# Performance work log

Hardware: AMD Instinct MI355X
Metric: run time of the kernel (lower is better)

Reference implementation:

```python
import jax, jax.numpy as jnp
import numpy as np

ALPHA = 0.2  # LeakyReLU negative slope


def setup_inputs() -> dict:
    key = jax.random.key(0)
    ks = jax.random.split(key, 7)
    B, Wn, K, E, O = 16, 64, 256, 128, 64
    s = lambda k, shape, fan: jax.random.normal(k, shape, jnp.float32) * (1.0 / np.sqrt(fan))
    return {
        "x": jax.random.normal(ks[0], (B, Wn, K), jnp.float32),
        "lin_w": s(ks[1], (E, 2 * Wn), 2 * Wn),   # torch Linear weight (out,in)
        "lin_b": jnp.zeros((E,), jnp.float32),
        "a": s(ks[2], (E,), E),
        "bias_kk": s(ks[3], (K, K), K) * 0.1,
        "fc_w": s(ks[4], (O, K), K),
        "fc_b": jnp.zeros((O,), jnp.float32),
    }


def reference(x, lin_w, lin_b, a, bias_kk, fc_w, fc_b):
    # x: (B, W, K) -> v: (B, K, W); K nodes, W features per node
    v = jnp.transpose(x, (0, 2, 1))
    Wn = v.shape[-1]
    # lin(concat(v_i, v_j)) == v_i @ W1^T + v_j @ W2^T + b  (avoids O(K^2*2W) concat)
    W1, W2 = lin_w[:, :Wn], lin_w[:, Wn:]
    left = jnp.einsum("bkw,ew->bke", v, W1)   # (B,K,E)
    right = jnp.einsum("bkw,ew->bke", v, W2)  # (B,K,E)
    g = left[:, :, None, :] + right[:, None, :, :] + lin_b  # (B,K,K,E)
    g = jnp.where(g >= 0, g, ALPHA * g)  # LeakyReLU
    e = jnp.einsum("bije,e->bij", g, a) + bias_kk  # (B,K,K)
    attn = jax.nn.softmax(e, axis=2)
    # dropout p=0.0 / eval mode -> identity
    h = jax.nn.sigmoid(jnp.einsum("bij,bjw->biw", attn, v))  # (B,K,W)
    out = jnp.einsum("bwk,ok->bwo", jnp.transpose(h, (0, 2, 1)), fc_w) + fc_b
    return out  # (B, W, out_dim)
```

## Files before the change

### kernel.cpp

```cpp
#include <hip/hip_runtime.h>
#include <hip/hip_bf16.h>

#define ALPHA 0.2f
#define C1 0.6f
#define C2 0.4f

typedef const __attribute__((address_space(1))) float gas_float;
typedef __attribute__((address_space(3))) float las_float;

__device__ __forceinline__ void gld_lds16(const float* g, float* l) {
  __builtin_amdgcn_global_load_lds((gas_float*)g, (las_float*)l, 16, 0, 0);
}

__global__ __launch_bounds__(256) void k_proj(
    const float* __restrict__ x, const float* __restrict__ lin_w,
    float* __restrict__ left, float* __restrict__ right, float* __restrict__ v) {
  const int xcd = blockIdx.x & 7;
  const int s   = blockIdx.x >> 3;
  const int b   = 2 * xcd + (s & 1);
  const int k0  = (s >> 1) * 8;
  const int tid = threadIdx.x;

  __shared__ float s_x[8][68];

  {
    const int w  = tid >> 2;
    const int kq = tid & 3;
    float2 xv = *(const float2*)(x + b * 16384 + w * 256 + k0 + kq * 2);
    s_x[kq * 2 + 0][w] = xv.x;
    s_x[kq * 2 + 1][w] = xv.y;
  }
  __syncthreads();

  if (tid < 128) {
    const int k  = tid >> 4;
    const int wq = tid & 15;
    float4 vv = *(const float4*)&s_x[k][wq * 4];
    *(float4*)(v + (b * 256 + k0 + k) * 64 + wq * 4) = vv;
  }

  const int e  = tid & 127;
  const int kh = tid >> 7;
  float accL[4] = {0, 0, 0, 0};
  float accR[4] = {0, 0, 0, 0};
  const float4* w1 = (const float4*)(lin_w + e * 128);
  const float4* w2 = w1 + 16;
#pragma unroll
  for (int wc = 0; wc < 16; ++wc) {
    float4 l = w1[wc];
    float4 r = w2[wc];
#pragma unroll
    for (int k = 0; k < 4; ++k) {
      float4 sx = *(const float4*)&s_x[kh * 4 + k][wc * 4];
      accL[k] += sx.x * l.x + sx.y * l.y + sx.z * l.z + sx.w * l.w;
      accR[k] += sx.x * r.x + sx.y * r.y + sx.z * r.z + sx.w * r.w;
    }
  }
#pragma unroll
  for (int k = 0; k < 4; ++k) {
    int kk = (b * 256 + k0 + kh * 4 + k) * 128 + e;
    left[kk]  = accL[k];
    right[kk] = accR[k];
  }
}

__global__ __launch_bounds__(256, 2) void k_attn(
    const float* __restrict__ left, const float* __restrict__ right,
    const float* __restrict__ lin_b, const float* __restrict__ a,
    const float* __restrict__ bias_kk, const float* __restrict__ v,
    float* __restrict__ h) {
  const int xcd = blockIdx.x & 7;
  const int sblk = blockIdx.x >> 3;
  const int b   = 2 * xcd + (sblk & 1);
  const int i0  = (sblk >> 1) * 8;
  const int tid = threadIdx.x;

  __shared__ float s_lb[8][132];
  __shared__ float s_a[128];
  __shared__ float s_ca[128];
  __shared__ float s_AL[8];
  __shared__ float s_sc[8][260];
  __shared__ float s_v[256][64];

  float bk[8];
#pragma unroll
  for (int i = 0; i < 8; ++i) bk[i] = bias_kk[(i0 + i) * 256 + tid];

  if (tid < 128) {
    float av = a[tid];
    s_a[tid]  = av;
    s_ca[tid] = C2 * av;
  }
  {
    const int ii = tid >> 5;
    const int e4 = (tid & 31) * 4;
    float4 lv = *(const float4*)(left + (b * 256 + i0 + ii) * 128 + e4);
    float4 bv = *(const float4*)(lin_b + e4);
    lv.x += bv.x; lv.y += bv.y; lv.z += bv.z; lv.w += bv.w;
    *(float4*)&s_lb[ii][e4] = lv;
  }
  __syncthreads();

  const float4* rp = (const float4*)(right + (b * 256 + tid) * 128);
  float4 r[32];
#pragma unroll
  for (int q = 0; q < 32; ++q) r[q] = rp[q];

  {
    const int seg0 = (tid >> 6) * 16;
    const int ln4  = (tid & 63) * 4;
    const float* vb = v + b * 16384;
#pragma unroll
    for (int t = 0; t < 16; ++t) {
      const int seg = seg0 + t;
      gld_lds16(vb + seg * 256 + ln4, &s_v[0][0] + seg * 256);
    }
  }

  {
    const int ii = tid >> 5, sl = tid & 31;
    float p = 0.f;
#pragma unroll
    for (int m = 0; m < 4; ++m) p += s_a[sl * 4 + m] * s_lb[ii][sl * 4 + m];
#pragma unroll
    for (int off = 16; off > 0; off >>= 1) p += __shfl_xor(p, off, 64);
    if (sl == 0) s_AL[ii] = p;
  }

  float acc[8];
#pragma unroll
  for (int i = 0; i < 8; ++i) acc[i] = 0.f;
  float ar = 0.f;
#pragma unroll
  for (int ec = 0; ec < 8; ++ec) {
    float4 r0 = r[ec * 4 + 0], r1 = r[ec * 4 + 1],
           r2 = r[ec * 4 + 2], r3 = r[ec * 4 + 3];
    float4 a0 = *(const float4*)&s_a[ec * 16 + 0];
    float4 a1 = *(const float4*)&s_a[ec * 16 + 4];
    float4 a2 = *(const float4*)&s_a[ec * 16 + 8];
    float4 a3 = *(const float4*)&s_a[ec * 16 + 12];
    ar += a0.x * r0.x + a0.y * r0.y + a0.z * r0.z + a0.w * r0.w;
    ar += a1.x * r1.x + a1.y * r1.y + a1.z * r1.z + a1.w * r1.w;
    ar += a2.x * r2.x + a2.y * r2.y + a2.z * r2.z + a2.w * r2.w;
    ar += a3.x * r3.x + a3.y * r3.y + a3.z * r3.z + a3.w * r3.w;
    float4 c0 = *(const float4*)&s_ca[ec * 16 + 0];
    float4 c1 = *(const float4*)&s_ca[ec * 16 + 4];
    float4 c2 = *(const float4*)&s_ca[ec * 16 + 8];
    float4 c3 = *(const float4*)&s_ca[ec * 16 + 12];
#pragma unroll
    for (int i = 0; i < 8; ++i) {
      float4 l0 = *(const float4*)&s_lb[i][ec * 16 + 0];
      float4 l1 = *(const float4*)&s_lb[i][ec * 16 + 4];
      float4 l2 = *(const float4*)&s_lb[i][ec * 16 + 8];
      float4 l3 = *(const float4*)&s_lb[i][ec * 16 + 12];
      float t, s = acc[i];
      t = l0.x + r0.x; s = fmaf(c0.x, fabsf(t), s);
      t = l0.y + r0.y; s = fmaf(c0.y, fabsf(t), s);
      t = l0.z + r0.z; s = fmaf(c0.z, fabsf(t), s);
      t = l0.w + r0.w; s = fmaf(c0.w, fabsf(t), s);
      t = l1.x + r1.x; s = fmaf(c1.x, fabsf(t), s);
      t = l1.y + r1.y; s = fmaf(c1.y, fabsf(t), s);
      t = l1.z + r1.z; s = fmaf(c1.z, fabsf(t), s);
      t = l1.w + r1.w; s = fmaf(c1.w, fabsf(t), s);
      t = l2.x + r2.x; s = fmaf(c2.x, fabsf(t), s);
      t = l2.y + r2.y; s = fmaf(c2.y, fabsf(t), s);
      t = l2.z + r2.z; s = fmaf(c2.z, fabsf(t), s);
      t = l2.w + r2.w; s = fmaf(c2.w, fabsf(t), s);
      t = l3.x + r3.x; s = fmaf(c3.x, fabsf(t), s);
      t = l3.y + r3.y; s = fmaf(c3.y, fabsf(t), s);
      t = l3.z + r3.z; s = fmaf(c3.z, fabsf(t), s);
      t = l3.w + r3.w; s = fmaf(c3.w, fabsf(t), s);
      acc[i] = s;
    }
  }
  __syncthreads();

#pragma unroll
  for (int i = 0; i < 8; ++i) {
    float sc = fmaf(C1, s_AL[i] + ar, acc[i]) + bk[i];
    s_sc[i][tid] = __expf(sc);
  }
  __syncthreads();

  float invA, invB;
  {
    const int wv = tid >> 6, lane = tid & 63;
    float sA = s_sc[2 * wv + 0][lane] + s_sc[2 * wv + 0][lane + 64] +
               s_sc[2 * wv + 0][lane + 128] + s_sc[2 * wv + 0][lane + 192];
    float sB = s_sc[2 * wv + 1][lane] + s_sc[2 * wv + 1][lane + 64] +
               s_sc[2 * wv + 1][lane + 128] + s_sc[2 * wv + 1][lane + 192];
#pragma unroll
    for (int off = 32; off > 0; off >>= 1) {
      sA += __shfl_xor(sA, off, 64);
      sB += __shfl_xor(sB, off, 64);
    }
    invA = 1.f / sA;
    invB = 1.f / sB;
  }

  const int iq = tid >> 5;
  const int w  = (tid & 31) * 2;
  float h0 = 0.f, h1 = 0.f;
#pragma unroll 4
  for (int jj = 0; jj < 256; jj += 4) {
    float4 at = *(const float4*)&s_sc[iq][jj];
    float2 v0 = *(const float2*)&s_v[jj + 0][w];
    float2 v1 = *(const float2*)&s_v[jj + 1][w];
    float2 v2 = *(const float2*)&s_v[jj + 2][w];
    float2 v3 = *(const float2*)&s_v[jj + 3][w];
    h0 += at.x * v0.x + at.y * v1.x + at.z * v2.x + at.w * v3.x;
    h1 += at.x * v0.y + at.y * v1.y + at.z * v2.y + at.w * v3.y;
  }
  const float inv = (iq & 1) ? invB : invA;
  float2 hv;
  hv.x = 1.f / (1.f + __expf(-h0 * inv));
  hv.y = 1.f / (1.f + __expf(-h1 * inv));
  *(float2*)(h + (b * 256 + i0 + iq) * 64 + w) = hv;
}

__global__ __launch_bounds__(256) void k_out(
    const float* __restrict__ h, const float* __restrict__ fc_w,
    const float* __restrict__ fc_b, float* __restrict__ out) {
  const int xcd = blockIdx.x & 7;
  const int s   = blockIdx.x >> 3;
  const int b   = 2 * xcd + (s & 1);
  const int wg  = s >> 1;
  const int wl  = threadIdx.x >> 6;
  const int o   = threadIdx.x & 63;
  const int w   = wg * 4 + wl;

  __shared__ float s_h[256 * 4];
  for (int idx = threadIdx.x; idx < 1024; idx += 256) {
    int k = idx >> 2, wl2 = idx & 3;
    s_h[idx] = h[(b * 256 + k) * 64 + wg * 4 + wl2];
  }
  __syncthreads();

  float acc = 0.f;
  const float4* fw = (const float4*)(fc_w + o * 256);
#pragma unroll
  for (int k4 = 0; k4 < 64; ++k4) {
    float4 f = fw[k4];
    int k = k4 * 4;
    acc += s_h[(k + 0) * 4 + wl] * f.x + s_h[(k + 1) * 4 + wl] * f.y +
           s_h[(k + 2) * 4 + wl] * f.z + s_h[(k + 3) * 4 + wl] * f.w;
  }
  out[b * 64 * 64 + w * 64 + o] = acc + fc_b[o];
}

extern "C" void kernel_launch(void* const* d_in, const int* in_sizes, int n_in,
                              void* d_out, int out_size, void* d_ws, size_t ws_size,
                              hipStream_t stream) {
  const float* x       = (const float*)d_in[0];
  const float* lin_w   = (const float*)d_in[1];
  const float* lin_b   = (const float*)d_in[2];
  const float* a       = (const float*)d_in[3];
  const float* bias_kk = (const float*)d_in[4];
  const float* fc_w    = (const float*)d_in[5];
  const float* fc_b    = (const float*)d_in[6];
  float* out = (float*)d_out;

  float* ws    = (float*)d_ws;
  float* left  = ws;
  float* right = ws + 524288;
  float* v     = ws + 1048576;
  float* h     = ws + 1310720;

  k_proj<<<512, 256, 0, stream>>>(x, lin_w, left, right, v);
  k_attn<<<512, 256, 0, stream>>>(left, right, lin_b, a, bias_kk, v, h);
  k_out<<<256, 256, 0, stream>>>(h, fc_w, fc_b, out);
}
```

Measured before the change: 108.4 us.

## Split attention block's embedding dimension across thread pairs with 512 threads

Doubles the k_attn block to 512 threads. Each pair of threads now handles one column j and splits the 128-wide embedding into two halves, combining partial sums with a lane shuffle. The attention-times-V stage is likewise split over two halves of j and reduced by shuffle. This halves the per-thread register array holding `right`, which should allow more waves per CU and more latency hiding. The cost is extra shuffles, redundant exp work on the inactive half, and a larger block sharing the same 66KB+ of LDS.

```diff
diff --git a/kernel.cpp b/kernel.cpp
--- a/kernel.cpp
+++ b/kernel.cpp
@@ -64,16 +64,18 @@
   }
 }
 
-__global__ __launch_bounds__(256, 2) void k_attn(
+__global__ __launch_bounds__(512, 4) void k_attn(
     const float* __restrict__ left, const float* __restrict__ right,
     const float* __restrict__ lin_b, const float* __restrict__ a,
     const float* __restrict__ bias_kk, const float* __restrict__ v,
     float* __restrict__ h) {
-  const int xcd = blockIdx.x & 7;
+  const int xcd  = blockIdx.x & 7;
   const int sblk = blockIdx.x >> 3;
-  const int b   = 2 * xcd + (sblk & 1);
-  const int i0  = (sblk >> 1) * 8;
-  const int tid = threadIdx.x;
+  const int b    = 2 * xcd + (sblk & 1);
+  const int i0   = (sblk >> 1) * 8;
+  const int tid  = threadIdx.x;
+  const int j    = tid >> 1;
+  const int eh   = tid & 1;
 
   __shared__ float s_lb[8][132];
   __shared__ float s_a[128];
@@ -82,48 +84,43 @@
   __shared__ float s_sc[8][260];
   __shared__ float s_v[256][64];
 
-  float bk[8];
-#pragma unroll
-  for (int i = 0; i < 8; ++i) bk[i] = bias_kk[(i0 + i) * 256 + tid];
-
   if (tid < 128) {
     float av = a[tid];
     s_a[tid]  = av;
     s_ca[tid] = C2 * av;
   }
   {
-    const int ii = tid >> 5;
-    const int e4 = (tid & 31) * 4;
-    float4 lv = *(const float4*)(left + (b * 256 + i0 + ii) * 128 + e4);
-    float4 bv = *(const float4*)(lin_b + e4);
-    lv.x += bv.x; lv.y += bv.y; lv.z += bv.z; lv.w += bv.w;
-    *(float4*)&s_lb[ii][e4] = lv;
-  }
-  __syncthreads();
-
-  const float4* rp = (const float4*)(right + (b * 256 + tid) * 128);
-  float4 r[32];
-#pragma unroll
-  for (int q = 0; q < 32; ++q) r[q] = rp[q];
-
-  {
-    const int seg0 = (tid >> 6) * 16;
+    const int ii = tid >> 6;
+    const int e2 = (tid & 63) * 2;
+    float2 lv = *(const float2*)(left + (b * 256 + i0 + ii) * 128 + e2);
+    float2 bv = *(const float2*)(lin_b + e2);
+    s_lb[ii][e2 + 0] = lv.x + bv.x;
+    s_lb[ii][e2 + 1] = lv.y + bv.y;
+  }
+  __syncthreads();
+
+  const float4* rp = (const float4*)(right + (b * 256 + j) * 128 + eh * 64);
+  float4 r[16];
+#pragma unroll
+  for (int q = 0; q < 16; ++q) r[q] = rp[q];
+
+  {
+    const int seg0 = (tid >> 6) * 8;
     const int ln4  = (tid & 63) * 4;
     const float* vb = v + b * 16384;
 #pragma unroll
-    for (int t = 0; t < 16; ++t) {
+    for (int t = 0; t < 8; ++t) {
       const int seg = seg0 + t;
       gld_lds16(vb + seg * 256 + ln4, &s_v[0][0] + seg * 256);
     }
   }
 
   {
-    const int ii = tid >> 5, sl = tid & 31;
-    float p = 0.f;
-#pragma unroll
-    for (int m = 0; m < 4; ++m) p += s_a[sl * 4 + m] * s_lb[ii][sl * 4 + m];
-#pragma unroll
-    for (int off = 16; off > 0; off >>= 1) p += __shfl_xor(p, off, 64);
+    const int ii = tid >> 6, sl = tid & 63;
+    float p = s_a[sl * 2] * s_lb[ii][sl * 2] +
+              s_a[sl * 2 + 1] * s_lb[ii][sl * 2 + 1];
+#pragma unroll
+    for (int off = 32; off > 0; off >>= 1) p += __shfl_xor(p, off, 64);
     if (sl == 0) s_AL[ii] = p;
   }
 
@@ -131,28 +128,30 @@
 #pragma unroll
   for (int i = 0; i < 8; ++i) acc[i] = 0.f;
   float ar = 0.f;
-#pragma unroll
-  for (int ec = 0; ec < 8; ++ec) {
+  const int eb = eh * 64;
+#pragma unroll
+  for (int ec = 0; ec < 4; ++ec) {
     float4 r0 = r[ec * 4 + 0], r1 = r[ec * 4 + 1],
            r2 = r[ec * 4 + 2], r3 = r[ec * 4 + 3];
-    float4 a0 = *(const float4*)&s_a[ec * 16 + 0];
-    float4 a1 = *(const float4*)&s_a[ec * 16 + 4];
-    float4 a2 = *(const float4*)&s_a[ec * 16 + 8];
-    float4 a3 = *(const float4*)&s_a[ec * 16 + 12];
+    const int base = eb + ec * 16;
+    float4 a0 = *(const float4*)&s_a[base + 0];
+    float4 a1 = *(const float4*)&s_a[base + 4];
+    float4 a2 = *(const float4*)&s_a[base + 8];
+    float4 a3 = *(const float4*)&s_a[base + 12];
     ar += a0.x * r0.x + a0.y * r0.y + a0.z * r0.z + a0.w * r0.w;
     ar += a1.x * r1.x + a1.y * r1.y + a1.z * r1.z + a1.w * r1.w;
     ar += a2.x * r2.x + a2.y * r2.y + a2.z * r2.z + a2.w * r2.w;
     ar += a3.x * r3.x + a3.y * r3.y + a3.z * r3.z + a3.w * r3.w;
-    float4 c0 = *(const float4*)&s_ca[ec * 16 + 0];
-    float4 c1 = *(const float4*)&s_ca[ec * 16 + 4];
-    float4 c2 = *(const float4*)&s_ca[ec * 16 + 8];
-    float4 c3 = *(const float4*)&s_ca[ec * 16 + 12];
+    float4 c0 = *(const float4*)&s_ca[base + 0];
+    float4 c1 = *(const float4*)&s_ca[base + 4];
+    float4 c2 = *(const float4*)&s_ca[base + 8];
+    float4 c3 = *(const float4*)&s_ca[base + 12];
 #pragma unroll
     for (int i = 0; i < 8; ++i) {
-      float4 l0 = *(const float4*)&s_lb[i][ec * 16 + 0];
-      float4 l1 = *(const float4*)&s_lb[i][ec * 16 + 4];
-      float4 l2 = *(const float4*)&s_lb[i][ec * 16 + 8];
-      float4 l3 = *(const float4*)&s_lb[i][ec * 16 + 12];
+      float4 l0 = *(const float4*)&s_lb[i][base + 0];
+      float4 l1 = *(const float4*)&s_lb[i][base + 4];
+      float4 l2 = *(const float4*)&s_lb[i][base + 8];
+      float4 l3 = *(const float4*)&s_lb[i][base + 12];
       float t, s = acc[i];
       t = l0.x + r0.x; s = fmaf(c0.x, fabsf(t), s);
       t = l0.y + r0.y; s = fmaf(c0.y, fabsf(t), s);
@@ -173,49 +172,59 @@
       acc[i] = s;
     }
   }
-  __syncthreads();
+
+  float bk[8];
+#pragma unroll
+  for (int i = 0; i < 8; ++i) bk[i] = bias_kk[(i0 + i) * 256 + j];
+
+  __syncthreads();
+
+#pragma unroll
+  for (int i = 0; i < 8; ++i) acc[i] += __shfl_xor(acc[i], 1, 64);
+  ar += __shfl_xor(ar, 1, 64);
 
 #pragma unroll
   for (int i = 0; i < 8; ++i) {
     float sc = fmaf(C1, s_AL[i] + ar, acc[i]) + bk[i];
-    s_sc[i][tid] = __expf(sc);
-  }
-  __syncthreads();
-
-  float invA, invB;
+    float p = __expf(sc);
+    if (eh == 0) s_sc[i][j] = p;
+  }
+  __syncthreads();
+
+  float inv;
   {
     const int wv = tid >> 6, lane = tid & 63;
-    float sA = s_sc[2 * wv + 0][lane] + s_sc[2 * wv + 0][lane + 64] +
-               s_sc[2 * wv + 0][lane + 128] + s_sc[2 * wv + 0][lane + 192];
-    float sB = s_sc[2 * wv + 1][lane] + s_sc[2 * wv + 1][lane + 64] +
-               s_sc[2 * wv + 1][lane + 128] + s_sc[2 * wv + 1][lane + 192];
-#pragma unroll
-    for (int off = 32; off > 0; off >>= 1) {
-      sA += __shfl_xor(sA, off, 64);
-      sB += __shfl_xor(sB, off, 64);
-    }
-    invA = 1.f / sA;
-    invB = 1.f / sB;
-  }
-
-  const int iq = tid >> 5;
-  const int w  = (tid & 31) * 2;
+    float ssum = s_sc[wv][lane] + s_sc[wv][lane + 64] +
+                 s_sc[wv][lane + 128] + s_sc[wv][lane + 192];
+#pragma unroll
+    for (int off = 32; off > 0; off >>= 1) ssum += __shfl_xor(ssum, off, 64);
+    inv = 1.f / ssum;
+  }
+
+  const int iq = tid >> 6;
+  const int wp = (tid >> 1) & 31;
+  const int jh = tid & 1;
+  const int w  = wp * 2;
   float h0 = 0.f, h1 = 0.f;
+  const int jbase = jh * 128;
 #pragma unroll 4
-  for (int jj = 0; jj < 256; jj += 4) {
-    float4 at = *(const float4*)&s_sc[iq][jj];
-    float2 v0 = *(const float2*)&s_v[jj + 0][w];
-    float2 v1 = *(const float2*)&s_v[jj + 1][w];
-    float2 v2 = *(const float2*)&s_v[jj + 2][w];
-    float2 v3 = *(const float2*)&s_v[jj + 3][w];
+  for (int jj = 0; jj < 128; jj += 4) {
+    float4 at = *(const float4*)&s_sc[iq][jbase + jj];
+    float2 v0 = *(const float2*)&s_v[jbase + jj + 0][w];
+    float2 v1 = *(const float2*)&s_v[jbase + jj + 1][w];
+    float2 v2 = *(const float2*)&s_v[jbase + jj + 2][w];
+    float2 v3 = *(const float2*)&s_v[jbase + jj + 3][w];
     h0 += at.x * v0.x + at.y * v1.x + at.z * v2.x + at.w * v3.x;
     h1 += at.x * v0.y + at.y * v1.y + at.z * v2.y + at.w * v3.y;
   }
-  const float inv = (iq & 1) ? invB : invA;
-  float2 hv;
-  hv.x = 1.f / (1.f + __expf(-h0 * inv));
-  hv.y = 1.f / (1.f + __expf(-h1 * inv));
-  *(float2*)(h + (b * 256 + i0 + iq) * 64 + w) = hv;
+  h0 += __shfl_xor(h0, 1, 64);
+  h1 += __shfl_xor(h1, 1, 64);
+  if (jh == 0) {
+    float2 hv;
+    hv.x = 1.f / (1.f + __expf(-h0 * inv));
+    hv.y = 1.f / (1.f + __expf(-h1 * inv));
+    *(float2*)(h + (b * 256 + i0 + iq) * 64 + w) = hv;
+  }
 }
 
 __global__ __launch_bounds__(256) void k_out(
@@ -267,6 +276,6 @@
   float* h     = ws + 1310720;
 
   k_proj<<<512, 256, 0, stream>>>(x, lin_w, left, right, v);
-  k_attn<<<512, 256, 0, stream>>>(left, right, lin_b, a, bias_kk, v, h);
+  k_attn<<<512, 512, 0, stream>>>(left, right, lin_b, a, bias_kk, v, h);
   k_out<<<256, 256, 0, stream>>>(h, fc_w, fc_b, out);
 }
```

After: 112.4 us. +3.7%, slower.
